# Kernel optimization log

Measured on AMD Instinct MI355X. Metric: run time of the kernel, lower is better.

## Reference

```python
import jax, jax.numpy as jnp
import numpy as np

DIM, HEADS, SEG, DIL = 1024, 16, 64, 2
B, L = 4, 4096
HEAD_DIM = DIM // HEADS
SCALE = HEAD_DIM ** -0.5


def _hilbert_map(seq_len: int) -> np.ndarray:
    # exact port of generate_hilbert_curve / hilbert_index
    size = int(np.ceil(np.sqrt(seq_len)))
    if size * size != seq_len:
        size = 2 ** int(np.ceil(np.log2(size)))

    def hidx(x, y, n):
        d = 0
        s = n // 2
        while s > 0:
            rx = 1 if (x & s) > 0 else 0
            ry = 1 if (y & s) > 0 else 0
            d += s * s * ((3 * rx) ^ ry)
            if ry == 0:
                if rx == 1:
                    x = n - 1 - x
                    y = n - 1 - y
                x, y = y, x
            s //= 2
        return d

    m = np.zeros(size * size, dtype=np.int32)
    for y in range(size):
        for x in range(size):
            m[y * size + x] = hidx(x, y, size)
    return m[:seq_len]


def setup_inputs() -> dict:
    key = jax.random.key(0)
    k1, k2, k3 = jax.random.split(key, 3)
    x = jax.random.normal(k1, (B, L, DIM), dtype=jnp.float32)
    w_qkv = jax.random.normal(k2, (DIM, 3 * DIM), dtype=jnp.float32) * 0.02
    w_proj = jax.random.normal(k3, (DIM, DIM), dtype=jnp.float32) * 0.02
    hilbert_map = jnp.asarray(_hilbert_map(L))
    return {"x": x, "w_qkv": w_qkv, "w_proj": w_proj, "hilbert_map": hilbert_map}


def reference(x, w_qkv, w_proj, hilbert_map):
    Bq, Lq, _ = x.shape
    n_seg = Lq // SEG
    # qkv projection -> [3, B, H, L, D]
    qkv = (x @ w_qkv).reshape(Bq, Lq, 3, HEADS, HEAD_DIM).transpose(2, 0, 3, 1, 4)
    q, k, v = qkv[0], qkv[1], qkv[2]
    # Hilbert reorder along sequence
    q = q[:, :, hilbert_map, :]
    k = k[:, :, hilbert_map, :]
    v = v[:, :, hilbert_map, :]
    # segmented dilated attention: [B,H,S,seg,D]
    qs = q.reshape(Bq, HEADS, n_seg, SEG, HEAD_DIM)
    ks = k.reshape(Bq, HEADS, n_seg, SEG, HEAD_DIM)[:, :, :, ::DIL, :]
    vs = v.reshape(Bq, HEADS, n_seg, SEG, HEAD_DIM)[:, :, :, ::DIL, :]
    scores = jnp.einsum('bhsqd,bhskd->bhsqk', qs, ks) * SCALE
    attn = jax.nn.softmax(scores, axis=-1)
    out = jnp.einsum('bhsqk,bhskd->bhsqd', attn, vs).reshape(Bq, HEADS, Lq, HEAD_DIM)
    # inverse Hilbert reorder
    inv = jnp.argsort(hilbert_map)
    out = out[:, :, inv, :]
    out = out.transpose(0, 2, 1, 3).reshape(Bq, Lq, DIM)
    return out @ w_proj
```

## Files before the change

kernel.cpp:

```cpp
#include <hip/hip_runtime.h>

#define L_SEQ 4096

typedef unsigned short u16;
typedef unsigned int u32;
typedef __bf16 bf16_t;
typedef bf16_t bf16x8 __attribute__((ext_vector_type(8)));
typedef float f32x4 __attribute__((ext_vector_type(4)));
typedef unsigned short u16x8 __attribute__((ext_vector_type(8)));
typedef unsigned short u16x4 __attribute__((ext_vector_type(4)));

__device__ __forceinline__ u16 f2b(float f) {
  unsigned u = __float_as_uint(f);
  u += 0x7fffu + ((u >> 16) & 1u);
  return (u16)(u >> 16);
}
__device__ __forceinline__ float b2f(u16 b) {
  return __uint_as_float(((unsigned)b) << 16);
}

#define FENCE asm volatile("" ::: "memory")
#define BARRIER __builtin_amdgcn_s_barrier()
#define WAIT_LGKM0 asm volatile("s_waitcnt lgkmcnt(0)" ::: "memory")
#define WAIT_VM4 asm volatile("s_waitcnt vmcnt(4)" ::: "memory")
#define SB0 __builtin_amdgcn_sched_barrier(0)
#define AS1 __attribute__((address_space(1)))
#define AS3 __attribute__((address_space(3)))

__global__ __launch_bounds__(256) void k_prep(const float* __restrict__ x,
                                              u16* __restrict__ xb,
                                              const float* __restrict__ wq,
                                              u16* __restrict__ wqT,
                                              const float* __restrict__ wp,
                                              u16* __restrict__ wpT) {
  const int bid = blockIdx.x;
  const int t = threadIdx.x;
  if (bid < 4096) {
    const int i = (bid * 256 + t) * 16;
    f32x4 v0 = *reinterpret_cast<const f32x4*>(x + i);
    f32x4 v1 = *reinterpret_cast<const f32x4*>(x + i + 4);
    f32x4 v2 = *reinterpret_cast<const f32x4*>(x + i + 8);
    f32x4 v3 = *reinterpret_cast<const f32x4*>(x + i + 12);
    u16x8 o0, o1;
#pragma unroll
    for (int j = 0; j < 4; ++j) {
      o0[j] = f2b(v0[j]); o0[4 + j] = f2b(v1[j]);
      o1[j] = f2b(v2[j]); o1[4 + j] = f2b(v3[j]);
    }
    *reinterpret_cast<u16x8*>(xb + i) = o0;
    *reinterpret_cast<u16x8*>(xb + i + 8) = o1;
    return;
  }
  const float* in; u16* out; int R, C, bx, by;
  if (bid < 7168) {
    const int b2 = bid - 4096;
    in = wq; out = wqT; R = 1024; C = 3072;
    bx = (b2 % 96) * 32; by = (b2 / 96) * 32;
  } else {
    const int b2 = bid - 7168;
    in = wp; out = wpT; R = 1024; C = 1024;
    bx = (b2 % 32) * 32; by = (b2 / 32) * 32;
  }
  __shared__ float tile[32][33];
  const int tx = t & 31, ty = t >> 5;
#pragma unroll
  for (int i = 0; i < 32; i += 8)
    tile[ty + i][tx] = in[(size_t)(by + ty + i) * C + (bx + tx)];
  __syncthreads();
#pragma unroll
  for (int i = 0; i < 32; i += 8)
    out[(size_t)(bx + ty + i) * R + (by + tx)] = f2b(tile[tx][ty + i]);
}

template <bool OUT_BF16>
__global__ __launch_bounds__(512, 2) void k_gemm256p(const u16* __restrict__ A,
                                                     const u16* __restrict__ Bt,
                                                     void* __restrict__ Cv,
                                                     int M, int N, int K,
                                                     int ntiles, int gx) {
  __shared__ __align__(16) char lds[131072];
  const int tid = threadIdx.x;
  const int wid = tid >> 6, lane = tid & 63;
  const int wm = wid >> 2, wn = wid & 3;
  const int lr = lane & 15, lq = lane >> 4;
  const int xr = (lr & 7) << 4;
  const int koff0 = (lq * 16) ^ xr;
  const int koff1 = (64 | (lq * 16)) ^ xr;

  const int cpx = 32 * ntiles;
  auto tilecoord = [&](int ff, int& mm, int& nn) {
    int swz = (ff & 7) * cpx + (ff >> 3);
    mm = (swz / gx) * 256; nn = (swz % gx) * 256;
  };

  const int rowT = tid >> 3;
  const int colT = (((tid * 16) & 127) ^ ((rowT & 7) << 4)) >> 1;
  const size_t r64K = (size_t)64 * K;
  const size_t r128K = (size_t)128 * K;

  int m0, n0;
  tilecoord(blockIdx.x, m0, n0);
  const u16* pAc = A + (size_t)(m0 + rowT) * K + colT;
  const u16* pBc = Bt + (size_t)(n0 + rowT) * K + colT;

  f32x4 acc[8][4];
  bf16x8 a[4][2];
  bf16x8 bb[2][2][2];

  auto STG = [&](const u16* bp, int region, size_t hoff, int k0) {
    const u16* s0 = bp + hoff + k0;
    __builtin_amdgcn_global_load_lds((const AS1 void*)s0,
                                     (AS3 void*)(lds + region + wid * 1024), 16, 0, 0);
    __builtin_amdgcn_global_load_lds((const AS1 void*)(s0 + r64K),
                                     (AS3 void*)(lds + region + 8192 + wid * 1024), 16, 0, 0);
  };
  auto rdA = [&](int dbuf, int mh) {
#pragma unroll
    for (int mi = 0; mi < 4; ++mi) {
      const int base = dbuf * 65536 + wm * 16384 + (mh * 64 + mi * 16 + lr) * 128;
      a[mi][0] = *(const bf16x8*)(lds + base + koff0);
      a[mi][1] = *(const bf16x8*)(lds + base + koff1);
    }
  };
  auto rdB = [&](int dbuf, int nh, int bset) {
#pragma unroll
    for (int ni = 0; ni < 2; ++ni) {
      const int base = dbuf * 65536 + 32768 + (wn >> 1) * 16384 +
                       ((wn & 1) * 64 + nh * 32 + ni * 16 + lr) * 128;
      bb[bset][ni][0] = *(const bf16x8*)(lds + base + koff0);
      bb[bset][ni][1] = *(const bf16x8*)(lds + base + koff1);
    }
  };
  auto mfma16 = [&](int mh, int nh, int bset) {
    __builtin_amdgcn_s_setprio(1);
#pragma unroll
    for (int kk = 0; kk < 2; ++kk)
#pragma unroll
      for (int ni = 0; ni < 2; ++ni)
#pragma unroll
        for (int mi = 0; mi < 4; ++mi)
          acc[mh * 4 + mi][nh * 2 + ni] = __builtin_amdgcn_mfma_f32_16x16x32_bf16(
              a[mi][kk], bb[bset][ni][kk], acc[mh * 4 + mi][nh * 2 + ni], 0, 0, 0);
    __builtin_amdgcn_s_setprio(0);
  };

  STG(pAc, 0,             0,     0);
  STG(pBc, 32768,         0,     0);
  STG(pBc, 49152,         r128K, 0);
  STG(pAc, 16384,         r128K, 0);
  STG(pBc, 65536 + 32768, 0,     64);
  STG(pBc, 65536 + 49152, r128K, 64);
  WAIT_VM4; FENCE; BARRIER;

  const int NT = K >> 6;
  const int NI = NT >> 1;

  for (int tt = 0; tt < ntiles; ++tt) {
    const bool hasn = (tt + 1 < ntiles);
    int m0n = m0, n0n = n0;
    if (hasn) tilecoord(blockIdx.x + (tt + 1) * 256, m0n, n0n);
    const u16* pAn = hasn ? (A + (size_t)(m0n + rowT) * K + colT) : pAc;
    const u16* pBn = hasn ? (Bt + (size_t)(n0n + rowT) * K + colT) : pBc;

    {
      f32x4 z = {0.f, 0.f, 0.f, 0.f};
#pragma unroll
      for (int i = 0; i < 8; ++i)
#pragma unroll
        for (int j = 0; j < 4; ++j) acc[i][j] = z;
    }

    for (int it = 0; it < NI; ++it) {
      const int kP1 = (2 * it + 1) * 64;
      const bool last = (it == NI - 1);
      const int kA = last ? 0 : (2 * it + 2) * 64;
      const int kB = last ? 64 : (2 * it + 3) * 64;
      const u16* sA = last ? pAn : pAc;
      const u16* sB = last ? pBn : pBc;

      rdA(0, 0); rdB(0, 0, 0);
      STG(pAc, 65536, 0, kP1);
      FENCE; BARRIER; WAIT_LGKM0; SB0;
      mfma16(0, 0, 0);
      FENCE; BARRIER;
      rdB(0, 1, 1);
      STG(pAc, 65536 + 16384, r128K, kP1);
      FENCE; BARRIER; WAIT_LGKM0; SB0;
      mfma16(0, 1, 1);
      FENCE; BARRIER;
      rdA(0, 1);
      STG(sB, 32768, 0, kA);
      STG(sB, 49152, r128K, kA);
      FENCE; BARRIER; WAIT_LGKM0; SB0;
      mfma16(1, 1, 1);
      mfma16(1, 0, 0);
      WAIT_VM4; FENCE; BARRIER;
      rdA(1, 0); rdB(1, 0, 0);
      STG(sA, 0, 0, kA);
      FENCE; BARRIER; WAIT_LGKM0; SB0;
      mfma16(0, 0, 0);
      FENCE; BARRIER;
      rdB(1, 1, 1);
      STG(sA, 16384, r128K, kA);
      FENCE; BARRIER; WAIT_LGKM0; SB0;
      mfma16(0, 1, 1);
      FENCE; BARRIER;
      rdA(1, 1);
      STG(sB, 65536 + 32768, 0, kB);
      STG(sB, 65536 + 49152, r128K, kB);
      FENCE; BARRIER; WAIT_LGKM0; SB0;
      mfma16(1, 1, 1);
      mfma16(1, 0, 0);
      WAIT_VM4; FENCE; BARRIER;
    }

#pragma unroll
    for (int mi = 0; mi < 8; ++mi)
#pragma unroll
      for (int ni = 0; ni < 4; ++ni) {
        const int r0 = m0 + wm * 128 + (mi >> 2) * 64 + (mi & 3) * 16 + lq * 4;
        const int c = n0 + wn * 64 + (ni >> 1) * 32 + (ni & 1) * 16 + lr;
#pragma unroll
        for (int r = 0; r < 4; ++r) {
          const float v = acc[mi][ni][r];
          if (OUT_BF16)
            ((u16*)Cv)[(size_t)(r0 + r) * N + c] = f2b(v);
          else
            ((float*)Cv)[(size_t)(r0 + r) * N + c] = v;
        }
      }

    m0 = m0n; n0 = n0n; pAc = pAn; pBc = pBn;
  }
}

__global__ __launch_bounds__(256) void k_attn2(const u16* __restrict__ qkv,
                                               const int* __restrict__ hmap,
                                               u16* __restrict__ att) {
  __shared__ u16 VT[64 * 40];
  __shared__ u16 Pl[4][16 * 40];

  const int blk = blockIdx.x;
  const int b = blk >> 10, h = (blk >> 6) & 15, s = blk & 63;
  const int t = threadIdx.x, w = t >> 6, lane = t & 63;
  const int lr = lane & 15, lq = lane >> 4;
  const int* hm = hmap + s * 64;
  const size_t bb = (size_t)b * L_SEQ;

  {
    const int kj = t >> 3, d0 = (t & 7) * 8;
    const u16* p = qkv + (bb + hm[2 * kj]) * 3072 + 2048 + h * 64 + d0;
    u16x8 v = *(const u16x8*)p;
#pragma unroll
    for (int j = 0; j < 8; ++j) {
      const int d = d0 + j;
      const int chunk = (kj >> 3) ^ ((d >> 3) & 3);
      VT[d * 40 + chunk * 8 + (kj & 7)] = v[j];
    }
  }

  const u16* qp = qkv + (bb + hm[16 * w + lr]) * 3072 + h * 64 + lq * 8;
  bf16x8 aq0 = *(const bf16x8*)(qp);
  bf16x8 aq1 = *(const bf16x8*)(qp + 32);
  bf16x8 bk[2][2];
#pragma unroll
  for (int nk = 0; nk < 2; ++nk) {
    const u16* kp = qkv + (bb + hm[2 * (nk * 16 + lr)]) * 3072 + 1024 + h * 64 + lq * 8;
    bk[nk][0] = *(const bf16x8*)(kp);
    bk[nk][1] = *(const bf16x8*)(kp + 32);
  }

  f32x4 z4 = {0.f, 0.f, 0.f, 0.f};
  f32x4 s0 = __builtin_amdgcn_mfma_f32_16x16x32_bf16(aq0, bk[0][0], z4, 0, 0, 0);
  s0 = __builtin_amdgcn_mfma_f32_16x16x32_bf16(aq1, bk[0][1], s0, 0, 0, 0);
  f32x4 s1 = __builtin_amdgcn_mfma_f32_16x16x32_bf16(aq0, bk[1][0], z4, 0, 0, 0);
  s1 = __builtin_amdgcn_mfma_f32_16x16x32_bf16(aq1, bk[1][1], s1, 0, 0, 0);

  float inv[4];
  u16* Pw = Pl[w];
#pragma unroll
  for (int r = 0; r < 4; ++r) {
    float a0 = s0[r] * 0.125f, a1 = s1[r] * 0.125f;
    float m = fmaxf(a0, a1);
    m = fmaxf(m, __shfl_xor(m, 1));
    m = fmaxf(m, __shfl_xor(m, 2));
    m = fmaxf(m, __shfl_xor(m, 4));
    m = fmaxf(m, __shfl_xor(m, 8));
    float e0 = __expf(a0 - m), e1 = __expf(a1 - m);
    float sum = e0 + e1;
    sum += __shfl_xor(sum, 1);
    sum += __shfl_xor(sum, 2);
    sum += __shfl_xor(sum, 4);
    sum += __shfl_xor(sum, 8);
    inv[r] = 1.f / sum;
    Pw[(lq * 4 + r) * 40 + lr] = f2b(e0);
    Pw[(lq * 4 + r) * 40 + 16 + lr] = f2b(e1);
  }

  __syncthreads();

  bf16x8 ap = *(const bf16x8*)(Pw + lr * 40 + lq * 8);
  f32x4 o[4];
#pragma unroll
  for (int nd = 0; nd < 4; ++nd) {
    const int row = nd * 16 + lr;
    const int chunk = lq ^ ((row >> 3) & 3);
    bf16x8 bv = *(const bf16x8*)(VT + row * 40 + chunk * 8);
    o[nd] = __builtin_amdgcn_mfma_f32_16x16x32_bf16(ap, bv, z4, 0, 0, 0);
  }

#pragma unroll
  for (int r = 0; r < 4; ++r) {
    u16* dst = att + (bb + hm[16 * w + lq * 4 + r]) * 1024 + h * 64 + lr;
#pragma unroll
    for (int nd = 0; nd < 4; ++nd)
      dst[nd * 16] = f2b(o[nd][r] * inv[r]);
  }
}

extern "C" void kernel_launch(void* const* d_in, const int* in_sizes, int n_in,
                              void* d_out, int out_size, void* d_ws, size_t ws_size,
                              hipStream_t stream) {
  const float* x = (const float*)d_in[0];
  const float* w_qkv = (const float*)d_in[1];
  const float* w_proj = (const float*)d_in[2];
  const int* hmap = (const int*)d_in[3];
  float* out = (float*)d_out;

  char* ws = (char*)d_ws;
  u16* qkvb  = (u16*)(ws);
  u16* xb    = (u16*)(ws + 100663296ull);
  u16* wqkvT = (u16*)(ws + 134217728ull);
  u16* wprojT= (u16*)(ws + 140509184ull);
  u16* att = xb;

  k_prep<<<8192, 256, 0, stream>>>(x, xb, w_qkv, wqkvT, w_proj, wprojT);
  k_gemm256p<true><<<256, 512, 0, stream>>>(xb, wqkvT, qkvb, 16384, 3072, 1024, 3, 12);
  k_attn2<<<4096, 256, 0, stream>>>(qkvb, hmap, att);
  k_gemm256p<false><<<256, 512, 0, stream>>>(att, wprojT, out, 16384, 1024, 1024, 1, 4);
}
```

Before: 189.3 us.

## Compute K/V projections only for dilated Hilbert-gathered tokens

Because attention only reads every second Hilbert-ordered key/value, the prep kernel now gathers and converts those x rows (half the tokens) into a compact bf16 buffer. The QKV GEMM splits into a Q GEMM over all tokens and a K/V GEMM over the gathered tokens, cutting the K/V projection FLOPs in half. The attention kernel then reads K/V contiguously per segment instead of through the Hilbert map. This adds a gather pass over x and splits the GEMM launch into mixed block types.

```diff
diff --git a/kernel.cpp b/kernel.cpp
--- a/kernel.cpp
+++ b/kernel.cpp
@@ -8,7 +8,6 @@
 typedef bf16_t bf16x8 __attribute__((ext_vector_type(8)));
 typedef float f32x4 __attribute__((ext_vector_type(4)));
 typedef unsigned short u16x8 __attribute__((ext_vector_type(8)));
-typedef unsigned short u16x4 __attribute__((ext_vector_type(4)));
 
 __device__ __forceinline__ u16 f2b(float f) {
   unsigned u = __float_as_uint(f);
@@ -32,7 +31,9 @@
                                               const float* __restrict__ wq,
                                               u16* __restrict__ wqT,
                                               const float* __restrict__ wp,
-                                              u16* __restrict__ wpT) {
+                                              u16* __restrict__ wpT,
+                                              const int* __restrict__ hmap,
+                                              u16* __restrict__ xg) {
   const int bid = blockIdx.x;
   const int t = threadIdx.x;
   if (bid < 4096) {
@@ -51,6 +52,26 @@
     *reinterpret_cast<u16x8*>(xb + i + 8) = o1;
     return;
   }
+  if (bid >= 8192) {
+    const int g = bid - 8192;
+    const int gi = g * 8 + (t >> 5);
+    const int lane32 = t & 31;
+    const int b = gi >> 11, i = gi & 2047;
+    const int s = i >> 5, j = i & 31;
+    const int token = hmap[s * 64 + 2 * j];
+    const float* src = x + ((size_t)(b * 4096 + token)) * 1024 + lane32 * 32;
+    u16* dst = xg + (size_t)gi * 1024 + lane32 * 32;
+#pragma unroll
+    for (int c = 0; c < 4; ++c) {
+      f32x4 v0 = *(const f32x4*)(src + c * 8);
+      f32x4 v1 = *(const f32x4*)(src + c * 8 + 4);
+      u16x8 o;
+#pragma unroll
+      for (int q = 0; q < 4; ++q) { o[q] = f2b(v0[q]); o[4 + q] = f2b(v1[q]); }
+      *(u16x8*)(dst + c * 8) = o;
+    }
+    return;
+  }
   const float* in; u16* out; int R, C, bx, by;
   if (bid < 7168) {
     const int b2 = bid - 4096;
@@ -73,12 +94,10 @@
 }
 
 template <bool OUT_BF16>
-__global__ __launch_bounds__(512, 2) void k_gemm256p(const u16* __restrict__ A,
-                                                     const u16* __restrict__ Bt,
-                                                     void* __restrict__ Cv,
-                                                     int M, int N, int K,
-                                                     int ntiles, int gx) {
-  __shared__ __align__(16) char lds[131072];
+__device__ __forceinline__ void gemm_body(char* lds, const u16* __restrict__ A,
+                                          const u16* __restrict__ Bt,
+                                          void* __restrict__ Cv,
+                                          int N, int K, int ntiles, int gx, int bid) {
   const int tid = threadIdx.x;
   const int wid = tid >> 6, lane = tid & 63;
   const int wm = wid >> 2, wn = wid & 3;
@@ -99,7 +118,7 @@
   const size_t r128K = (size_t)128 * K;
 
   int m0, n0;
-  tilecoord(blockIdx.x, m0, n0);
+  tilecoord(bid, m0, n0);
   const u16* pAc = A + (size_t)(m0 + rowT) * K + colT;
   const u16* pBc = Bt + (size_t)(n0 + rowT) * K + colT;
 
@@ -158,7 +177,7 @@
   for (int tt = 0; tt < ntiles; ++tt) {
     const bool hasn = (tt + 1 < ntiles);
     int m0n = m0, n0n = n0;
-    if (hasn) tilecoord(blockIdx.x + (tt + 1) * 256, m0n, n0n);
+    if (hasn) tilecoord(bid + (tt + 1) * 256, m0n, n0n);
     const u16* pAn = hasn ? (A + (size_t)(m0n + rowT) * K + colT) : pAc;
     const u16* pBn = hasn ? (Bt + (size_t)(n0n + rowT) * K + colT) : pBc;
 
@@ -234,7 +253,30 @@
   }
 }
 
-__global__ __launch_bounds__(256) void k_attn2(const u16* __restrict__ qkv,
+__global__ __launch_bounds__(512, 2) void k_gemm_qkv(const u16* __restrict__ xb,
+                                                     const u16* __restrict__ xg,
+                                                     const u16* __restrict__ wT,
+                                                     u16* __restrict__ qb,
+                                                     u16* __restrict__ kvb) {
+  __shared__ __align__(16) char lds[131072];
+  const bool kv = (blockIdx.x >= 256);
+  gemm_body<true>(lds,
+                  kv ? xg : xb,
+                  kv ? (wT + 1024 * 1024) : wT,
+                  kv ? (void*)kvb : (void*)qb,
+                  kv ? 2048 : 1024, 1024, 1, kv ? 8 : 4,
+                  blockIdx.x & 255);
+}
+
+__global__ __launch_bounds__(512, 2) void k_gemm_proj(const u16* __restrict__ A,
+                                                      const u16* __restrict__ Bt,
+                                                      float* __restrict__ C) {
+  __shared__ __align__(16) char lds[131072];
+  gemm_body<false>(lds, A, Bt, C, 1024, 1024, 1, 4, blockIdx.x);
+}
+
+__global__ __launch_bounds__(256) void k_attn2(const u16* __restrict__ qb,
+                                               const u16* __restrict__ kvb,
                                                const int* __restrict__ hmap,
                                                u16* __restrict__ att) {
   __shared__ u16 VT[64 * 40];
@@ -245,11 +287,12 @@
   const int t = threadIdx.x, w = t >> 6, lane = t & 63;
   const int lr = lane & 15, lq = lane >> 4;
   const int* hm = hmap + s * 64;
-  const size_t bb = (size_t)b * L_SEQ;
+  const size_t bb4 = (size_t)b * L_SEQ;
+  const size_t kvrow0 = (size_t)(b * 2048 + s * 32);
 
   {
     const int kj = t >> 3, d0 = (t & 7) * 8;
-    const u16* p = qkv + (bb + hm[2 * kj]) * 3072 + 2048 + h * 64 + d0;
+    const u16* p = kvb + (kvrow0 + kj) * 2048 + 1024 + h * 64 + d0;
     u16x8 v = *(const u16x8*)p;
 #pragma unroll
     for (int j = 0; j < 8; ++j) {
@@ -259,13 +302,13 @@
     }
   }
 
-  const u16* qp = qkv + (bb + hm[16 * w + lr]) * 3072 + h * 64 + lq * 8;
+  const u16* qp = qb + (bb4 + hm[16 * w + lr]) * 1024 + h * 64 + lq * 8;
   bf16x8 aq0 = *(const bf16x8*)(qp);
   bf16x8 aq1 = *(const bf16x8*)(qp + 32);
   bf16x8 bk[2][2];
 #pragma unroll
   for (int nk = 0; nk < 2; ++nk) {
-    const u16* kp = qkv + (bb + hm[2 * (nk * 16 + lr)]) * 3072 + 1024 + h * 64 + lq * 8;
+    const u16* kp = kvb + (kvrow0 + nk * 16 + lr) * 2048 + h * 64 + lq * 8;
     bk[nk][0] = *(const bf16x8*)(kp);
     bk[nk][1] = *(const bf16x8*)(kp + 32);
   }
@@ -311,7 +354,7 @@
 
 #pragma unroll
   for (int r = 0; r < 4; ++r) {
-    u16* dst = att + (bb + hm[16 * w + lq * 4 + r]) * 1024 + h * 64 + lr;
+    u16* dst = att + (bb4 + hm[16 * w + lq * 4 + r]) * 1024 + h * 64 + lr;
 #pragma unroll
     for (int nd = 0; nd < 4; ++nd)
       dst[nd * 16] = f2b(o[nd][r] * inv[r]);
@@ -328,14 +371,16 @@
   float* out = (float*)d_out;
 
   char* ws = (char*)d_ws;
-  u16* qkvb  = (u16*)(ws);
-  u16* xb    = (u16*)(ws + 100663296ull);
-  u16* wqkvT = (u16*)(ws + 134217728ull);
-  u16* wprojT= (u16*)(ws + 140509184ull);
+  u16* qb    = (u16*)(ws);
+  u16* kvb   = (u16*)(ws + 33554432ull);
+  u16* xb    = (u16*)(ws + 67108864ull);
+  u16* xg    = (u16*)(ws + 100663296ull);
+  u16* wqkvT = (u16*)(ws + 117440512ull);
+  u16* wpT   = (u16*)(ws + 123731968ull);
   u16* att = xb;
 
-  k_prep<<<8192, 256, 0, stream>>>(x, xb, w_qkv, wqkvT, w_proj, wprojT);
-  k_gemm256p<true><<<256, 512, 0, stream>>>(xb, wqkvT, qkvb, 16384, 3072, 1024, 3, 12);
-  k_attn2<<<4096, 256, 0, stream>>>(qkvb, hmap, att);
-  k_gemm256p<false><<<256, 512, 0, stream>>>(att, wprojT, out, 16384, 1024, 1024, 1, 4);
-}
+  k_prep<<<9216, 256, 0, stream>>>(x, xb, w_qkv, wqkvT, w_proj, wpT, hmap, xg);
+  k_gemm_qkv<<<512, 512, 0, stream>>>(xb, xg, wqkvT, qb, kvb);
+  k_attn2<<<4096, 256, 0, stream>>>(qb, kvb, hmap, att);
+  k_gemm_proj<<<256, 512, 0, stream>>>(att, wpT, out);
+}
```

Measured after the change: 166.5 us. 1.14x faster.
